# Kernel optimization log

Hardware: AMD Instinct MI355X
Metric: run time of the kernel (lower is better)

## Reference

```python
import jax, jax.numpy as jnp
import numpy as np

EMB = 768
HEADS = 8
HEAD_DIM = EMB // HEADS  # 96


def setup_inputs() -> dict:
    key = jax.random.key(0)
    ks = jax.random.split(key, 5)
    B, N = 4, 2048
    x = jax.random.normal(ks[0], (B, N, EMB), dtype=jnp.float32)
    s_in = 1.0 / np.sqrt(EMB)
    # weights stored as (in, out); equivalent to torch Linear y = x @ W + b
    w_qkv = jax.random.normal(ks[1], (EMB, 3 * EMB), dtype=jnp.float32) * s_in
    b_qkv = jax.random.normal(ks[2], (3 * EMB,), dtype=jnp.float32) * 0.02
    w_proj = jax.random.normal(ks[3], (EMB, EMB), dtype=jnp.float32) * s_in
    b_proj = jax.random.normal(ks[4], (EMB,), dtype=jnp.float32) * 0.02
    return {"x": x, "w_qkv": w_qkv, "b_qkv": b_qkv, "w_proj": w_proj, "b_proj": b_proj}


def reference(x, w_qkv, b_qkv, w_proj, b_proj):
    B, N, _ = x.shape
    qkv = x @ w_qkv + b_qkv  # [B, N, 3*EMB]
    # rearrange 'b n (h d qkv) -> qkv b h n d': qkv is the innermost split axis
    qkv = qkv.reshape(B, N, HEADS, HEAD_DIM, 3)
    qkv = jnp.transpose(qkv, (4, 0, 2, 1, 3))  # [3, B, H, N, D]
    q, k, v = qkv[0], qkv[1], qkv[2]
    inv_scale = 1.0 / np.sqrt(HEAD_DIM)  # applied AFTER softmax (faithful to source)
    scores = jnp.einsum('bhqd,bhkd->bhqk', q, k)
    attn = jax.nn.softmax(scores, axis=-1) * inv_scale
    out = jnp.einsum('bhqk,bhkd->bhqd', attn, v)
    out = jnp.transpose(out, (0, 2, 1, 3)).reshape(B, N, EMB)  # b h n d -> b n (h d)
    return out @ w_proj + b_proj
```

## Files before the change

kernel.cpp:

```cpp
#include <hip/hip_runtime.h>
#include <hip/hip_bf16.h>

#define EMB 768
#define NHEADS 8
#define HDIM 96
#define SEQ 2048
#define BATCH 4
#define QKV_COLS 2304
#define PB ((size_t)SEQ * EMB)

typedef _Float16 f16;
typedef _Float16 f16x8 __attribute__((ext_vector_type(8)));
typedef float f32x4 __attribute__((ext_vector_type(4)));

__device__ __forceinline__ void gl_lds16(const f16* g, f16* l) {
  __builtin_amdgcn_global_load_lds((const __attribute__((address_space(1))) void*)g,
                                   (__attribute__((address_space(3))) void*)l, 16, 0, 0);
}
__device__ __forceinline__ f32x4 shflx4(f32x4 v, int m) {
  f32x4 r;
  r[0] = __shfl_xor(v[0], m); r[1] = __shfl_xor(v[1], m);
  r[2] = __shfl_xor(v[2], m); r[3] = __shfl_xor(v[3], m);
  return r;
}
__device__ __forceinline__ f32x4 vmax4(f32x4 a, f32x4 b) {
  f32x4 r;
  r[0] = fmaxf(a[0], b[0]); r[1] = fmaxf(a[1], b[1]);
  r[2] = fmaxf(a[2], b[2]); r[3] = fmaxf(a[3], b[3]);
  return r;
}

__global__ __launch_bounds__(256) void conv_x8_k(const float* __restrict__ in, size_t in_off,
                                                 f16* __restrict__ out, int n8) {
  int i = blockIdx.x * 256 + threadIdx.x;
  if (i >= n8) return;
  const float4 a = *(const float4*)(in + in_off + (size_t)i * 8);
  const float4 b = *(const float4*)(in + in_off + (size_t)i * 8 + 4);
  f16x8 o;
  o[0] = (f16)a.x; o[1] = (f16)a.y; o[2] = (f16)a.z; o[3] = (f16)a.w;
  o[4] = (f16)b.x; o[5] = (f16)b.y; o[6] = (f16)b.z; o[7] = (f16)b.w;
  *(f16x8*)(out + (size_t)i * 8) = o;
}

__global__ __launch_bounds__(256) void wqkv_perm_k(const float* __restrict__ in,
                                                   f16* __restrict__ out) {
  int t = blockIdx.x * 256 + threadIdx.x;
  if (t >= QKV_COLS * (EMB / 8)) return;
  const int colp = t / (EMB / 8);
  const int r8 = (t - colp * (EMB / 8)) * 8;
  const int s = colp / 768, rem = colp - s * 768;
  const int h = rem / 96, d = rem - h * 96;
  const int c = h * 288 + d * 3 + s;
  f16x8 o;
#pragma unroll
  for (int i = 0; i < 8; i++) o[i] = (f16)in[(size_t)(r8 + i) * QKV_COLS + c];
  *(f16x8*)(out + (size_t)colp * EMB + r8) = o;
}

__global__ __launch_bounds__(256) void wproj_t_k(const float* __restrict__ in,
                                                 f16* __restrict__ out) {
  int t = blockIdx.x * 256 + threadIdx.x;
  if (t >= EMB * (EMB / 8)) return;
  const int cp = t / (EMB / 8);
  const int r8 = (t - cp * (EMB / 8)) * 8;
  f16x8 o;
#pragma unroll
  for (int i = 0; i < 8; i++) o[i] = (f16)in[(size_t)(r8 + i) * EMB + cp];
  *(f16x8*)(out + (size_t)cp * EMB + r8) = o;
}

__global__ __launch_bounds__(256) void bias_perm_k(const float* __restrict__ bq_in,
                                                   float* __restrict__ bq_out,
                                                   const float* __restrict__ bp_in,
                                                   float* __restrict__ bp_out) {
  int i = blockIdx.x * 256 + threadIdx.x;
  if (i < QKV_COLS) {
    const int s = i / 768, rem = i - s * 768;
    const int h = rem / 96, d = rem - h * 96;
    bq_out[i] = bq_in[h * 288 + d * 3 + s];
  }
  if (i < EMB) bp_out[i] = bp_in[i];
}

template<int MODE>
__global__ __launch_bounds__(256) void gemm_bt(
    const f16* __restrict__ A, const f16* __restrict__ Bt,
    const float* __restrict__ bias, float* __restrict__ Cout,
    f16* __restrict__ QK, f16* __restrict__ Vt,
    int M, int N, int Kd)
{
  __shared__ f16 smem[MODE == 1 ? 17408 : 8192];
  f16* sA = smem;
  f16* sB = smem + 4096;
  const int tid  = threadIdx.x;
  const int wave = tid >> 6, lane = tid & 63;
  const int quad = lane >> 4, l16 = lane & 15;
  const int tile_m = blockIdx.y * 128, tile_n = blockIdx.x * 128;
  const int wm = (wave >> 1) * 64, wn = (wave & 1) * 64;

  f32x4 acc[4][4];
  for (int i = 0; i < 4; i++)
    for (int j = 0; j < 4; j++)
      acc[i][j] = f32x4{0.f, 0.f, 0.f, 0.f};

  for (int k0 = 0; k0 < Kd; k0 += 32) {
    __syncthreads();
#pragma unroll
    for (int it = 0; it < 2; it++) {
      const int ch  = (it * 4 + wave) * 64 + lane;
      const int row = ch >> 2, c8 = (ch & 3) * 8;
      if (MODE == 2) {
        const int grow = tile_m + row;
        const int bb = grow >> 11, n = grow & 2047;
        const int hh = k0 / 96, d0 = k0 - hh * 96 + c8;
        gl_lds16(A + ((size_t)(bb * NHEADS + hh) * SEQ + n) * HDIM + d0,
                 &sA[(it * 4 + wave) * 512]);
      } else {
        gl_lds16(A + (size_t)(tile_m + row) * Kd + k0 + c8, &sA[(it * 4 + wave) * 512]);
      }
      gl_lds16(Bt + (size_t)(tile_n + row) * Kd + k0 + c8, &sB[(it * 4 + wave) * 512]);
    }
    __syncthreads();

    f16x8 af[4], bfr[4];
    for (int i = 0; i < 4; i++) af[i]  = *(const f16x8*)&sA[(wm + i * 16 + l16) * 32 + quad * 8];
    for (int j = 0; j < 4; j++) bfr[j] = *(const f16x8*)&sB[(wn + j * 16 + l16) * 32 + quad * 8];
    for (int i = 0; i < 4; i++)
      for (int j = 0; j < 4; j++)
        acc[i][j] = __builtin_amdgcn_mfma_f32_16x16x32_f16(af[i], bfr[j], acc[i][j], 0, 0, 0);
  }

  if (MODE == 1 && tile_n >= 1536) {
    __syncthreads();
    f16* sT = smem;
    for (int j = 0; j < 4; j++) {
      const int cl = wn + j * 16 + l16;
      const float bv = bias[tile_n + cl];
      for (int i = 0; i < 4; i++)
        for (int r = 0; r < 4; r++)
          sT[cl * 136 + wm + i * 16 + quad * 4 + r] = (f16)(acc[i][j][r] + bv);
    }
    __syncthreads();
    const int bb = tile_m >> 11;
    const int n0 = tile_m & 2047;
#pragma unroll
    for (int l = 0; l < 8; l++) {
      const int cc = l * 256 + tid;
      const int rh = cc >> 4, nof = (cc & 15) * 8;
      const int hd = (tile_n - 1536) + rh;
      const int h = hd / 96, d = hd - h * 96;
      f16x8 v = *(const f16x8*)&sT[rh * 136 + nof];
      *(f16x8*)(Vt + ((size_t)(bb * NHEADS + h) * HDIM + d) * SEQ + n0 + nof) = v;
    }
  } else {
    for (int j = 0; j < 4; j++) {
      const int col = tile_n + wn + j * 16 + l16;
      const float bv = bias[col];
      for (int i = 0; i < 4; i++) {
        for (int r = 0; r < 4; r++) {
          const int row = tile_m + wm + i * 16 + quad * 4 + r;
          const float fv = acc[i][j][r] + bv;
          if (MODE != 1) Cout[(size_t)row * N + col] = fv;
          else           QK  [(size_t)row * 1536 + col] = (f16)fv;
        }
      }
    }
  }
}

__global__ __launch_bounds__(256, 2) void attn_k(
    const f16* __restrict__ QK, const f16* __restrict__ Vt,
    f16* __restrict__ Out , int nbh)
{
  __shared__ f16 sK[128 * 96];
  __shared__ f16 sV[96 * 128];
  __shared__ f16 sP[128 * 64];
  const int tid  = threadIdx.x;
  const int wave = tid >> 6, lane = tid & 63;
  const int quad = lane >> 4, l16 = lane & 15;

  const int bid = blockIdx.x;
  const int xcd = bid & 7, idx = bid >> 3;
  const int bh  = xcd * (nbh >> 3) + (idx >> 4);
  const int qt  = idx & 15;
  const int b = bh >> 3, h = bh & 7;

  const int wrow = wave * 32;

  const f16* Qb = QK + (size_t)(b * SEQ + qt * 128 + wrow) * 1536 + h * 96;
  const f16* Kb = QK + (size_t)(b * SEQ) * 1536 + 768 + h * 96;
  const f16* Vb = Vt + (size_t)bh * HDIM * SEQ;

  f16x8 qf[2][3];
#pragma unroll
  for (int ti = 0; ti < 2; ti++)
#pragma unroll
    for (int kc = 0; kc < 3; kc++)
      qf[ti][kc] = *(const f16x8*)(Qb + (size_t)(ti * 16 + l16) * 1536 + kc * 32 + quad * 8);

  f32x4 oacc[2][6];
#pragma unroll
  for (int ti = 0; ti < 2; ti++)
#pragma unroll
    for (int dj = 0; dj < 6; dj++)
      oacc[ti][dj] = f32x4{0.f, 0.f, 0.f, 0.f};
  f32x4 m_run[2], l_run[2];
#pragma unroll
  for (int ti = 0; ti < 2; ti++) {
    m_run[ti] = f32x4{-1e30f, -1e30f, -1e30f, -1e30f};
    l_run[ti] = f32x4{0.f, 0.f, 0.f, 0.f};
  }

  for (int kt = 0; kt < SEQ / 128; kt++) {
    __syncthreads();
    {
      const f16* kt_base = Kb + (size_t)(kt * 128) * 1536;
      const f16* vt_base = Vb + kt * 128;
#pragma unroll
      for (int i = 0; i < 6; i++) {
        const int ck = i * 256 + tid;
        const int krow = ck / 12, ku = ck - krow * 12;
        *(uint4*)&sK[krow * 96 + ((ku + krow) % 12) * 8] =
            *(const uint4*)(kt_base + (size_t)krow * 1536 + ku * 8);
        const int cv = i * 256 + tid;
        const int vd = cv >> 4, vu = cv & 15;
        *(uint4*)&sV[vd * 128 + (vu ^ (vd & 15)) * 8] =
            *(const uint4*)(vt_base + (size_t)vd * SEQ + vu * 8);
      }
    }
    __syncthreads();

    f32x4 sacc[2][8];
#pragma unroll
    for (int ti = 0; ti < 2; ti++)
#pragma unroll
      for (int j = 0; j < 8; j++)
        sacc[ti][j] = f32x4{0.f, 0.f, 0.f, 0.f};
#pragma unroll
    for (int kc = 0; kc < 3; kc++) {
#pragma unroll
      for (int j = 0; j < 8; j++) {
        const int krow = j * 16 + l16;
        const f16x8 kf = *(const f16x8*)&sK[krow * 96 + ((kc * 4 + quad + krow) % 12) * 8];
        sacc[0][j] = __builtin_amdgcn_mfma_f32_16x16x32_f16(qf[0][kc], kf, sacc[0][j], 0, 0, 0);
        sacc[1][j] = __builtin_amdgcn_mfma_f32_16x16x32_f16(qf[1][kc], kf, sacc[1][j], 0, 0, 0);
      }
    }

    f32x4 rsv[2];
#pragma unroll
    for (int ti = 0; ti < 2; ti++) {
      f32x4 vmx = sacc[ti][0];
#pragma unroll
      for (int j = 1; j < 8; j++) vmx = vmax4(vmx, sacc[ti][j]);
      for (int m = 1; m < 16; m <<= 1) vmx = vmax4(vmx, shflx4(vmx, m));
      const f32x4 nm = vmax4(m_run[ti], vmx);
      f32x4 alpha;
      alpha[0] = __expf(m_run[ti][0] - nm[0]); alpha[1] = __expf(m_run[ti][1] - nm[1]);
      alpha[2] = __expf(m_run[ti][2] - nm[2]); alpha[3] = __expf(m_run[ti][3] - nm[3]);
      m_run[ti] = nm;
      l_run[ti] *= alpha;
      rsv[ti] = f32x4{0.f, 0.f, 0.f, 0.f};
#pragma unroll
      for (int dj = 0; dj < 6; dj++) oacc[ti][dj] *= alpha;
    }

#pragma unroll
    for (int c2 = 0; c2 < 2; c2++) {
#pragma unroll
      for (int ti = 0; ti < 2; ti++) {
        const int prow = wrow + ti * 16 + quad * 4;
#pragma unroll
        for (int jl = 0; jl < 4; jl++) {
          const int j = c2 * 4 + jl;
          f32x4 p;
          p[0] = __expf(sacc[ti][j][0] - m_run[ti][0]);
          p[1] = __expf(sacc[ti][j][1] - m_run[ti][1]);
          p[2] = __expf(sacc[ti][j][2] - m_run[ti][2]);
          p[3] = __expf(sacc[ti][j][3] - m_run[ti][3]);
          rsv[ti] += p;
          const int unit = jl * 2 + (l16 >> 3);
          const int within = l16 & 7;
#pragma unroll
          for (int rr = 0; rr < 4; rr++) {
            const int row = prow + rr;
            sP[row * 64 + (unit ^ (row & 7)) * 8 + within] = (f16)p[rr];
          }
        }
      }
#pragma unroll
      for (int kc2 = 0; kc2 < 2; kc2++) {
        const f16x8 pf0 = *(const f16x8*)&sP[(wrow + l16) * 64
                                            + ((kc2 * 4 + quad) ^ (l16 & 7)) * 8];
        const f16x8 pf1 = *(const f16x8*)&sP[(wrow + 16 + l16) * 64
                                            + ((kc2 * 4 + quad) ^ (l16 & 7)) * 8];
#pragma unroll
        for (int dj = 0; dj < 6; dj++) {
          const int vph = (c2 * 8 + kc2 * 4 + quad) ^ l16;
          const f16x8 vf = *(const f16x8*)&sV[(dj * 16 + l16) * 128 + vph * 8];
          oacc[0][dj] = __builtin_amdgcn_mfma_f32_16x16x32_f16(pf0, vf, oacc[0][dj], 0, 0, 0);
          oacc[1][dj] = __builtin_amdgcn_mfma_f32_16x16x32_f16(pf1, vf, oacc[1][dj], 0, 0, 0);
        }
      }
    }

#pragma unroll
    for (int ti = 0; ti < 2; ti++) {
      for (int m = 1; m < 16; m <<= 1) rsv[ti] += shflx4(rsv[ti], m);
      l_run[ti] += rsv[ti];
    }
  }

  const float inv_scale = 0.10206207261596577f;
#pragma unroll
  for (int ti = 0; ti < 2; ti++) {
#pragma unroll
    for (int r = 0; r < 4; r++) {
      const int qrow = qt * 128 + wrow + ti * 16 + quad * 4 + r;
      const float invl = inv_scale / l_run[ti][r];
      const size_t base = ((size_t)bh * SEQ + qrow) * HDIM;
#pragma unroll
      for (int dj = 0; dj < 6; dj++)
        Out[base + dj * 16 + l16] = (f16)(oacc[ti][dj][r] * invl);
    }
  }
}

extern "C" void kernel_launch(void* const* d_in, const int* in_sizes, int n_in,
                              void* d_out, int out_size, void* d_ws, size_t ws_size,
                              hipStream_t stream) {
  const float* x      = (const float*)d_in[0];
  const float* w_qkv  = (const float*)d_in[1];
  const float* b_qkv  = (const float*)d_in[2];
  const float* w_proj = (const float*)d_in[3];
  const float* b_proj = (const float*)d_in[4];
  float* outF = (float*)d_out;

  const size_t fixed = 256 + (size_t)QKV_COLS * EMB * 2 + (size_t)EMB * EMB * 2
                     + QKV_COLS * 4 + EMB * 4 + 256;
  const size_t perb = (size_t)4 * PB * 2;
  int nb = (ws_size >= fixed + 4 * perb) ? 4 : (ws_size >= fixed + 2 * perb) ? 2 : 1;

  char* ws = (char*)d_ws;
  ws += 256;
  f16*   wqkvT  = (f16*)ws;   ws += (size_t)QKV_COLS * EMB * 2;
  f16*   wprojT = (f16*)ws;   ws += (size_t)EMB * EMB * 2;
  float* bq     = (float*)ws; ws += (size_t)QKV_COLS * 4;
  float* bp     = (float*)ws; ws += (size_t)EMB * 4 + 256;
  f16* QK   = (f16*)ws;       ws += (size_t)nb * 2 * PB * 2;
  f16* Vt   = (f16*)ws;       ws += (size_t)nb * PB * 2;
  f16* attn = (f16*)ws;       ws += (size_t)nb * PB * 2;

  wqkv_perm_k<<<(QKV_COLS * (EMB / 8) + 255) / 256, 256, 0, stream>>>(w_qkv, wqkvT);
  wproj_t_k<<<(EMB * (EMB / 8) + 255) / 256, 256, 0, stream>>>(w_proj, wprojT);
  bias_perm_k<<<(QKV_COLS + 255) / 256, 256, 0, stream>>>(b_qkv, bq, b_proj, bp);

  for (int outer = 0; outer < BATCH / nb; outer++) {
    const int bbase = outer * nb;
    const size_t goff = (size_t)bbase * PB;
    f16* xg = (f16*)(outF + goff);
    const int n8 = (int)((size_t)nb * PB / 8);
    conv_x8_k<<<(n8 + 255) / 256, 256, 0, stream>>>(x, goff, xg, n8);

    dim3 g1(QKV_COLS / 128, nb * SEQ / 128);
    gemm_bt<1><<<g1, 256, 0, stream>>>(xg, wqkvT, bq, nullptr, QK, Vt,
                                       nb * SEQ, QKV_COLS, EMB);

    attn_k<<<dim3(16 * nb * NHEADS), 256, 0, stream>>>(QK, Vt, attn, nb * NHEADS);

    dim3 g3(EMB / 128, nb * SEQ / 128);
    gemm_bt<2><<<g3, 256, 0, stream>>>(attn, wprojT, bp, outF + goff,
                                       nullptr, nullptr,
                                       nb * SEQ, EMB, EMB);
  }
}
```

Before: 345.5 us.

## Pipeline K/V tile loads via direct global-to-LDS async copies in attention loop

Replaces the synchronous register-staged K/V tile loads with global_load_lds direct-to-LDS copies. Offsets are precomputed with an inverse swizzle so the existing LDS layout is kept. The next K tile is issued right after QK^T finishes and the next V tile right after PV, with vmcnt waits and barriers splitting each buffer's lifetime, so loads overlap with softmax and the MFMA work. This adds more barriers and relies on hand-counted vmcnt values and sched_barrier ordering, which risks hazards if the compiler emits other vector memory ops.

After: 330.2 us. 4.4% less time.

```diff
diff --git a/kernel.cpp b/kernel.cpp
--- a/kernel.cpp
+++ b/kernel.cpp
@@ -191,6 +191,17 @@
   const f16* Kb = QK + (size_t)(b * SEQ) * 1536 + 768 + h * 96;
   const f16* Vb = Vt + (size_t)bh * HDIM * SEQ;
 
+  int koff[6], voff[6];
+#pragma unroll
+  for (int i = 0; i < 6; i++) {
+    const int ck = i * 256 + tid;
+    const int krow = ck / 12, pu = ck - krow * 12;
+    const int u = (pu + 12 - krow % 12) % 12;
+    koff[i] = krow * 1536 + u * 8;
+    const int vd = ck >> 4, pv = ck & 15;
+    voff[i] = vd * SEQ + (pv ^ (vd & 15)) * 8;
+  }
+
   f16x8 qf[2][3];
 #pragma unroll
   for (int ti = 0; ti < 2; ti++)
@@ -211,24 +222,21 @@
     l_run[ti] = f32x4{0.f, 0.f, 0.f, 0.f};
   }
 
-  for (int kt = 0; kt < SEQ / 128; kt++) {
-    __syncthreads();
-    {
-      const f16* kt_base = Kb + (size_t)(kt * 128) * 1536;
-      const f16* vt_base = Vb + kt * 128;
-#pragma unroll
-      for (int i = 0; i < 6; i++) {
-        const int ck = i * 256 + tid;
-        const int krow = ck / 12, ku = ck - krow * 12;
-        *(uint4*)&sK[krow * 96 + ((ku + krow) % 12) * 8] =
-            *(const uint4*)(kt_base + (size_t)krow * 1536 + ku * 8);
-        const int cv = i * 256 + tid;
-        const int vd = cv >> 4, vu = cv & 15;
-        *(uint4*)&sV[vd * 128 + (vu ^ (vd & 15)) * 8] =
-            *(const uint4*)(vt_base + (size_t)vd * SEQ + vu * 8);
-      }
-    }
-    __syncthreads();
+  {
+    const f16* kb = Kb;
+    const f16* vb = Vb;
+#pragma unroll
+    for (int i = 0; i < 6; i++) gl_lds16(kb + koff[i], &sK[(i * 256 + wave * 64) * 8]);
+#pragma unroll
+    for (int i = 0; i < 6; i++) gl_lds16(vb + voff[i], &sV[(i * 256 + wave * 64) * 8]);
+  }
+
+  const int NT = SEQ / 128;
+  for (int kt = 0; kt < NT; kt++) {
+    if (kt == 0) asm volatile("s_waitcnt vmcnt(0)" ::: "memory");
+    else         asm volatile("s_waitcnt vmcnt(6)" ::: "memory");
+    __builtin_amdgcn_s_barrier();
+    __builtin_amdgcn_sched_barrier(0);
 
     f32x4 sacc[2][8];
 #pragma unroll
@@ -246,6 +254,15 @@
         sacc[1][j] = __builtin_amdgcn_mfma_f32_16x16x32_f16(qf[1][kc], kf, sacc[1][j], 0, 0, 0);
       }
     }
+
+    __builtin_amdgcn_sched_barrier(0);
+    __builtin_amdgcn_s_barrier();
+    if (kt < NT - 1) {
+      const f16* kb = Kb + (size_t)((kt + 1) * 128) * 1536;
+#pragma unroll
+      for (int i = 0; i < 6; i++) gl_lds16(kb + koff[i], &sK[(i * 256 + wave * 64) * 8]);
+    }
+    __builtin_amdgcn_sched_barrier(0);
 
     f32x4 rsv[2];
 #pragma unroll
@@ -264,6 +281,11 @@
 #pragma unroll
       for (int dj = 0; dj < 6; dj++) oacc[ti][dj] *= alpha;
     }
+
+    if (kt < NT - 1) asm volatile("s_waitcnt vmcnt(6)" ::: "memory");
+    else             asm volatile("s_waitcnt vmcnt(0)" ::: "memory");
+    __builtin_amdgcn_s_barrier();
+    __builtin_amdgcn_sched_barrier(0);
 
 #pragma unroll
     for (int c2 = 0; c2 < 2; c2++) {
@@ -304,6 +326,15 @@
       }
     }
 
+    __builtin_amdgcn_sched_barrier(0);
+    __builtin_amdgcn_s_barrier();
+    if (kt < NT - 1) {
+      const f16* vb = Vb + (kt + 1) * 128;
+#pragma unroll
+      for (int i = 0; i < 6; i++) gl_lds16(vb + voff[i], &sV[(i * 256 + wave * 64) * 8]);
+    }
+    __builtin_amdgcn_sched_barrier(0);
+
 #pragma unroll
     for (int ti = 0; ti < 2; ti++) {
       for (int m = 1; m < 16; m <<= 1) rsv[ti] += shflx4(rsv[ti], m);
```
